# Optimization experiments

Measured on AMD Instinct MI355X. Metric: run time of the kernel, lower is better.

The kernel has to match this reference:

```python
import jax, jax.numpy as jnp
import numpy as np

TEMP = 0.1        # ds_temperature
THRESHOLD = 0.2
MARGIN = 2        # margin_remove


def setup_inputs() -> dict:
    key = jax.random.key(0)
    k0, k1 = jax.random.split(key)
    N, C = 2, 256
    h0, w0, h1, w1 = 60, 80, 60, 80
    feature0 = jax.random.normal(k0, (N, h0 * w0, C), dtype=jnp.float32)
    feature1 = jax.random.normal(k1, (N, h1 * w1, C), dtype=jnp.float32)
    return {"feature0": feature0, "feature1": feature1,
            "h0": h0, "w0": w0, "h1": h1, "w1": w1}


def _interior(n: int, b: int) -> jnp.ndarray:
    # True on [b, n-b), mirroring mask[:, :b]=False and mask[:, -b:]=False
    a = jnp.arange(n)
    return (a >= b) & (a < n - b)


def reference(feature0, feature1, h0, w0, h1, w1):
    N, L, C = feature0.shape
    S = feature1.shape[1]
    # similarities: (f0/sqrt(C)) . (f1/sqrt(C)) / temp == f0.f1 / (C*temp)
    sim = jnp.einsum('nlc,nsc->nls', feature0, feature1) / (C * TEMP)
    # dual softmax confidences
    conf = jax.nn.softmax(sim, axis=2) * jax.nn.softmax(sim, axis=1)
    # threshold mask with spatial margin removal (mask0 is None branch)
    mask = conf > THRESHOLD                      # [N, L, S]
    m5 = mask.reshape(N, h0, w0, h1, w1)
    valid = (_interior(h0, MARGIN)[:, None, None, None]
             & _interior(w0, MARGIN)[None, :, None, None]
             & _interior(h1, MARGIN)[None, None, :, None]
             & _interior(w1, MARGIN)[None, None, None, :])
    m5 = m5 & valid[None]
    mask = m5.reshape(N, L, S)
    # mutual nearest neighbor constraint
    mutual = ((conf == conf.max(axis=2, keepdims=True))
              & (conf == conf.max(axis=1, keepdims=True)))
    mask = mask & mutual
    # dense (jit-safe) encoding of the matches: confidences zeroed off-match.
    matched_conf = jnp.where(mask, conf, 0.0)
    return conf, mask, matched_conf
```

## Files before the change

### kernel.cpp

```cpp
#include <hip/hip_runtime.h>

#define NB 2
#define LD 4800
#define SD 4800
#define CD 256
#define H0 60
#define W0 80
#define H1 60
#define W1 80
#define MG 2
#define THRESH 0.2f
#define SIM_SCALE (1.0f / (256.0f * 0.1f))
#define GT 38
#define CAP 8192

typedef float f32x4 __attribute__((ext_vector_type(4)));
typedef __bf16 bf16x8 __attribute__((ext_vector_type(8)));
typedef unsigned short u16x8 __attribute__((ext_vector_type(8)));

#define GLOBAL_AS __attribute__((address_space(1)))
#define LDS_AS __attribute__((address_space(3)))

__device__ __forceinline__ void gl_lds16(const unsigned short* g, unsigned short* l) {
    __builtin_amdgcn_global_load_lds((const GLOBAL_AS unsigned int*)g,
                                     (LDS_AS unsigned int*)l, 16, 0, 0);
}

__device__ __forceinline__ unsigned short f2bf(float f) {
    unsigned int u = __float_as_uint(f);
    u = u + 0x7FFFu + ((u >> 16) & 1u);
    return (unsigned short)(u >> 16);
}

__device__ __forceinline__ bool interior0(int idx) {
    int i = idx / W0, j = idx % W0;
    return (i >= MG) & (i < H0 - MG) & (j >= MG) & (j < W0 - MG);
}
__device__ __forceinline__ bool interior1(int idx) {
    int i = idx / W1, j = idx % W1;
    return (i >= MG) & (i < H1 - MG) & (j >= MG) & (j < W1 - MG);
}

__global__ __launch_bounds__(256) void k_prep(float* __restrict__ p, int n) {
    int i = blockIdx.x * 256 + threadIdx.x;
    if (i < n) p[i] = 0.f;
}

__global__ __launch_bounds__(256) void k_cvt(const float* __restrict__ src,
                                             unsigned short* __restrict__ dst, int n8) {
    int i = blockIdx.x * 256 + threadIdx.x;
    if (i >= n8) return;
    const float4* s = (const float4*)src + (size_t)i * 2;
    float4 a = s[0], b = s[1];
    u16x8 o = {f2bf(a.x), f2bf(a.y), f2bf(a.z), f2bf(a.w),
               f2bf(b.x), f2bf(b.y), f2bf(b.z), f2bf(b.w)};
    *(u16x8*)(dst + (size_t)i * 8) = o;
}

template <int PASS>
__global__ __launch_bounds__(256) void k_gemm(const unsigned short* __restrict__ bA,
                                              const unsigned short* __restrict__ bB,
                                              float* __restrict__ rowsum,
                                              float* __restrict__ colsum,
                                              float* __restrict__ conf,
                                              unsigned int* __restrict__ rowmax,
                                              unsigned int* __restrict__ colmax,
                                              unsigned int* __restrict__ cnt,
                                              uint4* __restrict__ list) {
    __shared__ __align__(16) unsigned short As[128][32];
    __shared__ __align__(16) unsigned short Bs[128][32];

    const int n  = blockIdx.z;
    const int s0 = blockIdx.x * 128;
    const int l0 = blockIdx.y * 128;
    const int tid  = threadIdx.x;
    const int lane = tid & 63;
    const int wave = tid >> 6;
    const int wm = (wave >> 1) * 64;
    const int wn = (wave & 1) * 64;
    const int quad = lane >> 4;
    const int lr   = lane & 15;

    const int sr = wave * 32 + (lane >> 2);
    const int sc = (lane & 3) * 8;
    const unsigned short* ga0 = bA + ((size_t)n * LD + min(l0 + sr,      LD - 1)) * CD + sc;
    const unsigned short* ga1 = bA + ((size_t)n * LD + min(l0 + sr + 16, LD - 1)) * CD + sc;
    const unsigned short* gb0 = bB + ((size_t)n * SD + min(s0 + sr,      SD - 1)) * CD + sc;
    const unsigned short* gb1 = bB + ((size_t)n * SD + min(s0 + sr + 16, SD - 1)) * CD + sc;
    unsigned short* la0 = &As[wave * 32][0];
    unsigned short* la1 = &As[wave * 32 + 16][0];
    unsigned short* lb0 = &Bs[wave * 32][0];
    unsigned short* lb1 = &Bs[wave * 32 + 16][0];

    f32x4 acc[4][4];
#pragma unroll
    for (int i = 0; i < 4; ++i)
#pragma unroll
        for (int j = 0; j < 4; ++j) acc[i][j] = (f32x4){0.f, 0.f, 0.f, 0.f};

    for (int k0 = 0; k0 < CD; k0 += 32) {
        __syncthreads();
        gl_lds16(ga0 + k0, la0);
        gl_lds16(ga1 + k0, la1);
        gl_lds16(gb0 + k0, lb0);
        gl_lds16(gb1 + k0, lb1);
        __syncthreads();

        bf16x8 af[4], bfr[4];
#pragma unroll
        for (int i = 0; i < 4; ++i) {
            af[i]  = __builtin_bit_cast(bf16x8, *(const u16x8*)&As[wm + i * 16 + lr][quad * 8]);
            bfr[i] = __builtin_bit_cast(bf16x8, *(const u16x8*)&Bs[wn + i * 16 + lr][quad * 8]);
        }
#pragma unroll
        for (int i = 0; i < 4; ++i)
#pragma unroll
            for (int j = 0; j < 4; ++j)
                acc[i][j] = __builtin_amdgcn_mfma_f32_16x16x32_bf16(af[i], bfr[j], acc[i][j], 0, 0, 0);
    }

    const int rb = l0 + wm;
    const int cb = s0 + wn;

    if (PASS == 0) {
        float rpart[4][4];
        float cpart[4];
#pragma unroll
        for (int i = 0; i < 4; ++i) {
            cpart[i] = 0.f;
#pragma unroll
            for (int g = 0; g < 4; ++g) rpart[i][g] = 0.f;
        }
#pragma unroll
        for (int mi = 0; mi < 4; ++mi)
#pragma unroll
            for (int ni = 0; ni < 4; ++ni)
#pragma unroll
                for (int g = 0; g < 4; ++g) {
                    int row = rb + mi * 16 + quad * 4 + g;
                    int col = cb + ni * 16 + lr;
                    float sv = acc[mi][ni][g] * SIM_SCALE;
                    bool ok = (row < LD) & (col < SD);
                    float ev = ok ? __expf(sv) : 0.f;
                    rpart[mi][g] += ev;
                    cpart[ni] += ev;
                }
#pragma unroll
        for (int mi = 0; mi < 4; ++mi)
#pragma unroll
            for (int g = 0; g < 4; ++g) {
                float v = rpart[mi][g];
                v += __shfl_xor(v, 1);
                v += __shfl_xor(v, 2);
                v += __shfl_xor(v, 4);
                v += __shfl_xor(v, 8);
                int row = rb + mi * 16 + quad * 4 + g;
                if (lr == 0 && row < LD) atomicAdd(&rowsum[n * LD + row], v);
            }
#pragma unroll
        for (int ni = 0; ni < 4; ++ni) {
            float v = cpart[ni];
            v += __shfl_xor(v, 16);
            v += __shfl_xor(v, 32);
            int col = cb + ni * 16 + lr;
            if (quad == 0 && col < SD) atomicAdd(&colsum[n * SD + col], v);
        }
    } else {
        float rinv[4][4], cinv[4];
#pragma unroll
        for (int mi = 0; mi < 4; ++mi)
#pragma unroll
            for (int g = 0; g < 4; ++g) {
                int row = min(rb + mi * 16 + quad * 4 + g, LD - 1);
                rinv[mi][g] = 1.0f / rowsum[n * LD + row];
            }
#pragma unroll
        for (int ni = 0; ni < 4; ++ni) {
            int col = min(cb + ni * 16 + lr, SD - 1);
            cinv[ni] = 1.0f / colsum[n * SD + col];
        }
#pragma unroll
        for (int mi = 0; mi < 4; ++mi)
#pragma unroll
            for (int ni = 0; ni < 4; ++ni)
#pragma unroll
                for (int g = 0; g < 4; ++g) {
                    int row = rb + mi * 16 + quad * 4 + g;
                    int col = cb + ni * 16 + lr;
                    float sv = acc[mi][ni][g] * SIM_SCALE;
                    float e = __expf(sv);
                    float cv = e * e * rinv[mi][g] * cinv[ni];
                    bool ok = (row < LD) & (col < SD);
                    if (ok) {
                        conf[((size_t)n * LD + row) * SD + col] = cv;
                        if (cv > THRESH) {
                            atomicMax(&rowmax[n * LD + row], __float_as_uint(cv));
                            atomicMax(&colmax[n * SD + col], __float_as_uint(cv));
                            unsigned int id = atomicAdd(cnt, 1u);
                            if (id < CAP) {
                                uint4 rec = {(unsigned)n, (unsigned)row, (unsigned)col,
                                             __float_as_uint(cv)};
                                list[id] = rec;
                            }
                        }
                    }
                }
    }
}

__global__ __launch_bounds__(256) void k_fillz(float4* __restrict__ p, size_t n4) {
    size_t i = (size_t)blockIdx.x * 256 + threadIdx.x;
    const size_t stride = (size_t)gridDim.x * 256;
    const float4 z = {0.f, 0.f, 0.f, 0.f};
    for (; i < n4; i += stride) p[i] = z;
}

__global__ __launch_bounds__(256) void k_fix(const unsigned int* __restrict__ cnt,
                                             const uint4* __restrict__ list,
                                             const unsigned int* __restrict__ rowmax,
                                             const unsigned int* __restrict__ colmax,
                                             float* __restrict__ mask,
                                             float* __restrict__ matched) {
    unsigned int m = min(*cnt, (unsigned int)CAP);
    for (unsigned int i = threadIdx.x; i < m; i += 256) {
        uint4 r = list[i];
        int n = (int)r.x, row = (int)r.y, col = (int)r.z;
        unsigned int cb = r.w;
        if (cb == rowmax[n * LD + row] && cb == colmax[n * SD + col] &&
            interior0(row) && interior1(col)) {
            size_t o = ((size_t)n * LD + row) * SD + col;
            mask[o] = 1.f;
            matched[o] = __uint_as_float(cb);
        }
    }
}

extern "C" void kernel_launch(void* const* d_in, const int* in_sizes, int n_in,
                              void* d_out, int out_size, void* d_ws, size_t ws_size,
                              hipStream_t stream) {
    const float* f0 = (const float*)d_in[0];
    const float* f1 = (const float*)d_in[1];
    const size_t plane = (size_t)NB * LD * SD;
    float* conf = (float*)d_out;
    float* mask = conf + plane;

    float* rowsum = (float*)d_ws;
    float* colsum = rowsum + NB * LD;
    unsigned int* rowmaxu = (unsigned int*)(colsum + NB * SD);
    unsigned int* colmaxu = rowmaxu + NB * LD;
    unsigned int* cnt = colmaxu + NB * SD;
    uint4* list = (uint4*)(cnt + 4);
    unsigned short* bf0 = (unsigned short*)(list + CAP);
    unsigned short* bf1 = bf0 + (size_t)NB * LD * CD;

    const int nz = NB * (LD + SD) * 2 + 4;
    k_prep<<<dim3((nz + 255) / 256), 256, 0, stream>>>(rowsum, nz);
    const int n8 = NB * LD * CD / 8;
    k_cvt<<<dim3((n8 + 255) / 256), 256, 0, stream>>>(f0, bf0, n8);
    k_cvt<<<dim3((n8 + 255) / 256), 256, 0, stream>>>(f1, bf1, n8);

    dim3 gg(GT, GT, NB);
    k_gemm<0><<<gg, 256, 0, stream>>>(bf0, bf1, rowsum, colsum, nullptr,
                                      nullptr, nullptr, nullptr, nullptr);
    k_gemm<1><<<gg, 256, 0, stream>>>(bf0, bf1, rowsum, colsum, conf,
                                      rowmaxu, colmaxu, cnt, list);
    k_fillz<<<dim3(4096), 256, 0, stream>>>((float4*)mask, 2 * plane / 4);
    k_fix<<<dim3(1), 256, 0, stream>>>(cnt, list, rowmaxu, colmaxu, mask, mask + plane);
}
```

Baseline: 691.3 us.

## Replace recomputing second GEMM pass with stored exponentials and separate normalize pass

The GEMM now runs once. It accumulates the row and column exp sums and also writes the unnormalized exp(sim)^2 into the conf buffer. A small kernel then inverts the sums, and a new elementwise kernel scales conf by the row and column inverses. That kernel also zeroes the mask and matched planes and records above-threshold candidates with their row and column maxima. This removes the second full GEMM recompute but adds an extra read and write of the large conf plane, trading compute for memory traffic.

New measurement: 708.0 us. 2.4% more time.

```diff
diff --git a/kernel.cpp b/kernel.cpp
--- a/kernel.cpp
+++ b/kernel.cpp
@@ -57,16 +57,11 @@
     *(u16x8*)(dst + (size_t)i * 8) = o;
 }
 
-template <int PASS>
 __global__ __launch_bounds__(256) void k_gemm(const unsigned short* __restrict__ bA,
                                               const unsigned short* __restrict__ bB,
                                               float* __restrict__ rowsum,
                                               float* __restrict__ colsum,
-                                              float* __restrict__ conf,
-                                              unsigned int* __restrict__ rowmax,
-                                              unsigned int* __restrict__ colmax,
-                                              unsigned int* __restrict__ cnt,
-                                              uint4* __restrict__ list) {
+                                              float* __restrict__ conf) {
     __shared__ __align__(16) unsigned short As[128][32];
     __shared__ __align__(16) unsigned short Bs[128][32];
 
@@ -122,97 +117,104 @@
     const int rb = l0 + wm;
     const int cb = s0 + wn;
 
-    if (PASS == 0) {
-        float rpart[4][4];
-        float cpart[4];
-#pragma unroll
-        for (int i = 0; i < 4; ++i) {
-            cpart[i] = 0.f;
-#pragma unroll
-            for (int g = 0; g < 4; ++g) rpart[i][g] = 0.f;
-        }
-#pragma unroll
-        for (int mi = 0; mi < 4; ++mi)
-#pragma unroll
-            for (int ni = 0; ni < 4; ++ni)
-#pragma unroll
-                for (int g = 0; g < 4; ++g) {
-                    int row = rb + mi * 16 + quad * 4 + g;
-                    int col = cb + ni * 16 + lr;
-                    float sv = acc[mi][ni][g] * SIM_SCALE;
-                    bool ok = (row < LD) & (col < SD);
-                    float ev = ok ? __expf(sv) : 0.f;
-                    rpart[mi][g] += ev;
-                    cpart[ni] += ev;
-                }
-#pragma unroll
-        for (int mi = 0; mi < 4; ++mi)
+    float rpart[4][4];
+    float cpart[4];
+#pragma unroll
+    for (int i = 0; i < 4; ++i) {
+        cpart[i] = 0.f;
+#pragma unroll
+        for (int g = 0; g < 4; ++g) rpart[i][g] = 0.f;
+    }
+#pragma unroll
+    for (int mi = 0; mi < 4; ++mi)
+#pragma unroll
+        for (int ni = 0; ni < 4; ++ni)
 #pragma unroll
             for (int g = 0; g < 4; ++g) {
-                float v = rpart[mi][g];
-                v += __shfl_xor(v, 1);
-                v += __shfl_xor(v, 2);
-                v += __shfl_xor(v, 4);
-                v += __shfl_xor(v, 8);
                 int row = rb + mi * 16 + quad * 4 + g;
-                if (lr == 0 && row < LD) atomicAdd(&rowsum[n * LD + row], v);
+                int col = cb + ni * 16 + lr;
+                float sv = acc[mi][ni][g] * SIM_SCALE;
+                bool ok = (row < LD) & (col < SD);
+                float ev = ok ? __expf(sv) : 0.f;
+                rpart[mi][g] += ev;
+                cpart[ni] += ev;
+                if (ok) conf[((size_t)n * LD + row) * SD + col] = ev * ev;
             }
 #pragma unroll
-        for (int ni = 0; ni < 4; ++ni) {
-            float v = cpart[ni];
-            v += __shfl_xor(v, 16);
-            v += __shfl_xor(v, 32);
-            int col = cb + ni * 16 + lr;
-            if (quad == 0 && col < SD) atomicAdd(&colsum[n * SD + col], v);
-        }
-    } else {
-        float rinv[4][4], cinv[4];
-#pragma unroll
-        for (int mi = 0; mi < 4; ++mi)
-#pragma unroll
-            for (int g = 0; g < 4; ++g) {
-                int row = min(rb + mi * 16 + quad * 4 + g, LD - 1);
-                rinv[mi][g] = 1.0f / rowsum[n * LD + row];
-            }
-#pragma unroll
-        for (int ni = 0; ni < 4; ++ni) {
-            int col = min(cb + ni * 16 + lr, SD - 1);
-            cinv[ni] = 1.0f / colsum[n * SD + col];
-        }
-#pragma unroll
-        for (int mi = 0; mi < 4; ++mi)
-#pragma unroll
-            for (int ni = 0; ni < 4; ++ni)
-#pragma unroll
-                for (int g = 0; g < 4; ++g) {
-                    int row = rb + mi * 16 + quad * 4 + g;
-                    int col = cb + ni * 16 + lr;
-                    float sv = acc[mi][ni][g] * SIM_SCALE;
-                    float e = __expf(sv);
-                    float cv = e * e * rinv[mi][g] * cinv[ni];
-                    bool ok = (row < LD) & (col < SD);
-                    if (ok) {
-                        conf[((size_t)n * LD + row) * SD + col] = cv;
-                        if (cv > THRESH) {
-                            atomicMax(&rowmax[n * LD + row], __float_as_uint(cv));
-                            atomicMax(&colmax[n * SD + col], __float_as_uint(cv));
-                            unsigned int id = atomicAdd(cnt, 1u);
-                            if (id < CAP) {
-                                uint4 rec = {(unsigned)n, (unsigned)row, (unsigned)col,
-                                             __float_as_uint(cv)};
-                                list[id] = rec;
-                            }
-                        }
+    for (int mi = 0; mi < 4; ++mi)
+#pragma unroll
+        for (int g = 0; g < 4; ++g) {
+            float v = rpart[mi][g];
+            v += __shfl_xor(v, 1);
+            v += __shfl_xor(v, 2);
+            v += __shfl_xor(v, 4);
+            v += __shfl_xor(v, 8);
+            int row = rb + mi * 16 + quad * 4 + g;
+            if (lr == 0 && row < LD) atomicAdd(&rowsum[n * LD + row], v);
+        }
+#pragma unroll
+    for (int ni = 0; ni < 4; ++ni) {
+        float v = cpart[ni];
+        v += __shfl_xor(v, 16);
+        v += __shfl_xor(v, 32);
+        int col = cb + ni * 16 + lr;
+        if (quad == 0 && col < SD) atomicAdd(&colsum[n * SD + col], v);
+    }
+}
+
+__global__ __launch_bounds__(256) void k_inv(float* __restrict__ p, int n) {
+    int i = blockIdx.x * 256 + threadIdx.x;
+    if (i < n) p[i] = 1.0f / p[i];
+}
+
+__global__ __launch_bounds__(256) void k_norm(f32x4* __restrict__ conf4,
+                                              const float* __restrict__ rinv,
+                                              const float* __restrict__ cinv,
+                                              f32x4* __restrict__ mask4,
+                                              f32x4* __restrict__ match4,
+                                              unsigned int* __restrict__ rowmax,
+                                              unsigned int* __restrict__ colmax,
+                                              unsigned int* __restrict__ cnt,
+                                              uint4* __restrict__ list) {
+    const int SD4 = SD / 4;
+    const size_t total = (size_t)NB * LD * SD4;
+    size_t i = (size_t)blockIdx.x * 256 + threadIdx.x;
+    const size_t stride = (size_t)gridDim.x * 256;
+    const f32x4 z = {0.f, 0.f, 0.f, 0.f};
+    for (; i < total; i += stride) {
+        int r  = (int)(i / SD4);
+        int c4 = (int)(i % SD4);
+        int nn = r / LD;
+        float ri = rinv[r];
+        f32x4 cf = *(const f32x4*)(cinv + nn * SD + c4 * 4);
+        f32x4 e2 = conf4[i];
+        f32x4 cv;
+        cv[0] = e2[0] * ri * cf[0];
+        cv[1] = e2[1] * ri * cf[1];
+        cv[2] = e2[2] * ri * cf[2];
+        cv[3] = e2[3] * ri * cf[3];
+        conf4[i]  = cv;
+        mask4[i]  = z;
+        match4[i] = z;
+        if (cv[0] > THRESH || cv[1] > THRESH || cv[2] > THRESH || cv[3] > THRESH) {
+            int l = r - nn * LD;
+#pragma unroll
+            for (int j = 0; j < 4; ++j) {
+                float v = cv[j];
+                if (v > THRESH) {
+                    int col = c4 * 4 + j;
+                    unsigned int vb = __float_as_uint(v);
+                    atomicMax(&rowmax[r], vb);
+                    atomicMax(&colmax[nn * SD + col], vb);
+                    unsigned int id = atomicAdd(cnt, 1u);
+                    if (id < CAP) {
+                        uint4 rec = {(unsigned)nn, (unsigned)l, (unsigned)col, vb};
+                        list[id] = rec;
                     }
                 }
-    }
-}
-
-__global__ __launch_bounds__(256) void k_fillz(float4* __restrict__ p, size_t n4) {
-    size_t i = (size_t)blockIdx.x * 256 + threadIdx.x;
-    const size_t stride = (size_t)gridDim.x * 256;
-    const float4 z = {0.f, 0.f, 0.f, 0.f};
-    for (; i < n4; i += stride) p[i] = z;
+            }
+        }
+    }
 }
 
 __global__ __launch_bounds__(256) void k_fix(const unsigned int* __restrict__ cnt,
@@ -260,10 +262,13 @@
     k_cvt<<<dim3((n8 + 255) / 256), 256, 0, stream>>>(f1, bf1, n8);
 
     dim3 gg(GT, GT, NB);
-    k_gemm<0><<<gg, 256, 0, stream>>>(bf0, bf1, rowsum, colsum, nullptr,
-                                      nullptr, nullptr, nullptr, nullptr);
-    k_gemm<1><<<gg, 256, 0, stream>>>(bf0, bf1, rowsum, colsum, conf,
-                                      rowmaxu, colmaxu, cnt, list);
-    k_fillz<<<dim3(4096), 256, 0, stream>>>((float4*)mask, 2 * plane / 4);
+    k_gemm<<<gg, 256, 0, stream>>>(bf0, bf1, rowsum, colsum, conf);
+
+    const int ninv = NB * (LD + SD);
+    k_inv<<<dim3((ninv + 255) / 256), 256, 0, stream>>>(rowsum, ninv);
+
+    k_norm<<<dim3(2048), 256, 0, stream>>>((f32x4*)conf, rowsum, colsum,
+                                           (f32x4*)mask, (f32x4*)(mask + plane),
+                                           rowmaxu, colmaxu, cnt, list);
     k_fix<<<dim3(1), 256, 0, stream>>>(cnt, list, rowmaxu, colmaxu, mask, mask + plane);
 }
```
